# Optimization experiments

Hardware: AMD Instinct MI355X
Metric: run time of the kernel (lower is better)

## Reference

```python
import jax, jax.numpy as jnp
import numpy as np

P = 8          # patch_size
DIM = 256      # embed dim
HEADS = 8
HEAD_DIM = DIM // HEADS
CH = 3
PATCH_DIM = CH * P * P  # 192
INNER = int(4.0 * DIM)  # 1024
SCALE = HEAD_DIM ** -0.5


def sine_pos_embedding(n, c, dtype=jnp.float32):
    # standard 1D sinusoidal position encoding, shape (n, c)
    pos = jnp.arange(n, dtype=jnp.float32)[:, None]            # (n,1)
    div = jnp.exp(jnp.arange(0, c, 2, dtype=jnp.float32) * (-np.log(10000.0) / c))
    pe = jnp.zeros((n, c), dtype=jnp.float32)
    pe = pe.at[:, 0::2].set(jnp.sin(pos * div))
    pe = pe.at[:, 1::2].set(jnp.cos(pos * div))
    return pe.astype(dtype)


def patchify(x):
    # (B,C,H,W) -> (B, n, p1*p2*C), matching 'b c (h p1) (w p2) -> b (h w) (p1 p2 c)'
    B, C, H, W = x.shape
    hp, wp = H // P, W // P
    x = x.reshape(B, C, hp, P, wp, P)
    x = x.transpose(0, 2, 4, 3, 5, 1)        # (B, hp, wp, p1, p2, C)
    return x.reshape(B, hp * wp, P * P * C)


def unpatchify(x, hp, wp):
    # (B, n, p1*p2*C) -> (B, C, H, W)
    B = x.shape[0]
    x = x.reshape(B, hp, wp, P, P, CH)
    x = x.transpose(0, 5, 1, 3, 2, 4)        # (B, C, hp, p1, wp, p2)
    return x.reshape(B, CH, hp * P, wp * P)


def setup_inputs() -> dict:
    key = jax.random.key(0)
    ks = jax.random.split(key, 16)
    B, H, W = 8, 256, 256
    s = 0.02
    img0 = jax.random.normal(ks[0], (B, CH, H, W), dtype=jnp.float32)
    img1 = jax.random.normal(ks[1], (B, CH, H, W), dtype=jnp.float32)
    mask = jax.random.randint(ks[2], (B, 1, H, W), 0, 2).astype(jnp.float32)
    return {
        "img0": img0,
        "img1": img1,
        "mask": mask,
        "w_patch": jax.random.normal(ks[3], (PATCH_DIM, DIM), jnp.float32) * s,
        "b_patch": jnp.zeros((DIM,), jnp.float32),
        "w_kv": jax.random.normal(ks[4], (DIM, 2 * DIM), jnp.float32) * s,
        "b_kv": jnp.zeros((2 * DIM,), jnp.float32),
        "w_qv": jax.random.normal(ks[5], (DIM, 2 * DIM), jnp.float32) * s,
        "b_qv": jnp.zeros((2 * DIM,), jnp.float32),
        "w_fc1": jax.random.normal(ks[6], (DIM, INNER), jnp.float32) * s,
        "b_fc1": jnp.zeros((INNER,), jnp.float32),
        "w_fc2": jax.random.normal(ks[7], (INNER, PATCH_DIM), jnp.float32) * s,
        "b_fc2": jnp.zeros((PATCH_DIM,), jnp.float32),
    }


def reference(img0, img1, mask, w_patch, b_patch, w_kv, b_kv, w_qv, b_qv,
              w_fc1, b_fc1, w_fc2, b_fc2):
    B, C, H, W = img0.shape
    hp, wp = H // P, W // P
    n = hp * wp

    x0 = patchify(img0) @ w_patch + b_patch   # (B, n, dim)
    x1 = patchify(img1) @ w_patch + b_patch
    pe = sine_pos_embedding(n, DIM)
    x0 = x0 + pe
    x1 = x1 + pe

    # img0 -> k, v
    kv = (x0 @ w_kv + b_kv).reshape(B, n, 2, HEADS, HEAD_DIM)
    kv = kv.transpose(2, 0, 3, 1, 4)          # (2, B, heads, n, hd)
    k, v = kv[0], kv[1]

    # img1 -> q (v1 unused in forward, matching torch code)
    qv = (x1 @ w_qv + b_qv).reshape(B, n, 2, DIM).transpose(2, 0, 1, 3)
    q = qv[0].reshape(B, n, HEADS, HEAD_DIM).transpose(0, 2, 1, 3)  # (B, heads, n, hd)

    dots = jnp.einsum('bhqd,bhkd->bhqk', q, k) * SCALE  # (B, heads, n, n)

    # mask: (B,1,H,W) -> per-patch sum -> binary -> additive bias over key dim
    msum = mask.reshape(B, 1, hp, P, wp, P).sum(axis=(3, 5)).reshape(B, 1, n)
    bias = jnp.where(msum > 0, 0.0, -100.0)[:, :, None, :]  # (B,1,1,n)

    attn = jax.nn.softmax(dots + bias, axis=-1)
    out = jnp.einsum('bhqk,bhkd->bhqd', attn, v)
    out = out.transpose(0, 2, 1, 3).reshape(B, n, DIM)

    # mlp2: Linear -> GELU(exact) -> Linear
    h = jax.nn.gelu(out @ w_fc1 + b_fc1, approximate=False)
    res = h @ w_fc2 + b_fc2                   # (B, n, patch_dim)

    return unpatchify(res, hp, wp)            # (B, C, H, W)
```

## Files before the change

kernel.cpp:

```cpp
#include <hip/hip_runtime.h>
#include <cstdint>
#include <cstddef>

typedef __bf16 bf16_t;
typedef __bf16 bf16x8 __attribute__((ext_vector_type(8)));
typedef float f32x4 __attribute__((ext_vector_type(4)));

__device__ __forceinline__ void gload_lds16(const bf16_t* g, bf16_t* l) {
  __builtin_amdgcn_global_load_lds((const __attribute__((address_space(1))) void*)g,
                                   (__attribute__((address_space(3))) void*)l,
                                   16, 0, 0);
}

__device__ __forceinline__ f32x4 mfma16(bf16x8 a, bf16x8 b, f32x4 c) {
  return __builtin_amdgcn_mfma_f32_16x16x32_bf16(a, b, c, 0, 0, 0);
}

__global__ __launch_bounds__(256)
void prep_all(const float* __restrict__ img0, const float* __restrict__ img1,
              const float* __restrict__ mask,
              const float* __restrict__ wp, const float* __restrict__ wkv,
              const float* __restrict__ wqv, const float* __restrict__ wfc1,
              const float* __restrict__ wfc2,
              bf16_t* __restrict__ xp0, bf16_t* __restrict__ xp1,
              float* __restrict__ pe, float* __restrict__ bias,
              bf16_t* __restrict__ wpT, bf16_t* __restrict__ wkvT,
              bf16_t* __restrict__ wqT, bf16_t* __restrict__ wfc1T,
              bf16_t* __restrict__ wfc2T) {
  int bid = blockIdx.x, tid = threadIdx.x;
  if (bid < 1536) {
    int imgsel = bid >= 768;
    int t = (bid - (imgsel ? 768 : 0)) * 256 + tid;
    const float* img = imgsel ? img1 : img0;
    bf16_t* xp = imgsel ? xp1 : xp0;
    int wpp = t & 31, p1 = (t >> 5) & 7, hp = (t >> 8) & 31, rest = t >> 13;
    int b = rest / 3, c = rest - b * 3;
    const float* src = img + (((size_t)(b * 3 + c) * 256 + hp * 8 + p1) * 256 + wpp * 8);
    float4 v0 = *(const float4*)src;
    float4 v1 = *(const float4*)(src + 4);
    int row = b * 1024 + hp * 32 + wpp;
    bf16_t* dst = xp + (size_t)row * 192 + p1 * 24 + c;
    dst[0]  = (bf16_t)v0.x; dst[3]  = (bf16_t)v0.y; dst[6]  = (bf16_t)v0.z; dst[9]  = (bf16_t)v0.w;
    dst[12] = (bf16_t)v1.x; dst[15] = (bf16_t)v1.y; dst[18] = (bf16_t)v1.z; dst[21] = (bf16_t)v1.w;
  } else if (bid < 4544) {
    int g = (bid - 1536) * 256 + tid;
    if (g < 49152) {
      int idx = g; int n = idx / 192, k = idx - n * 192;
      wpT[idx] = (bf16_t)wp[k * 256 + n];
    } else if (g < 180224) {
      int idx = g - 49152; int n = idx >> 8, k = idx & 255;
      wkvT[idx] = (bf16_t)wkv[k * 512 + n];
    } else if (g < 245760) {
      int idx = g - 180224; int n = idx >> 8, k = idx & 255;
      wqT[idx] = (bf16_t)wqv[k * 512 + n];
    } else if (g < 507904) {
      int idx = g - 245760; int n = idx >> 8, k = idx & 255;
      wfc1T[idx] = (bf16_t)wfc1[k * 1024 + n];
    } else if (g < 770048) {
      int idx = g - 507904; int n = idx >> 10, k = idx & 1023;
      wfc2T[idx] = (n < 192) ? (bf16_t)wfc2[k * 192 + n] : (bf16_t)0.0f;
    }
  } else if (bid < 5568) {
    int t = bid - 4544, c = tid;
    int i2 = c & ~1;
    float div = expf((float)i2 * (-9.210340371976184f / 256.0f));
    float arg = (float)t * div;
    pe[t * 256 + c] = (c & 1) ? cosf(arg) : sinf(arg);
  } else {
    int g = (bid - 5568) * 256 + tid;
    int b = g >> 10, t = g & 1023, hp = t >> 5, wpp = t & 31;
    const float* mp = mask + ((size_t)b * 256 + hp * 8) * 256 + wpp * 8;
    float s = 0.f;
    #pragma unroll
    for (int p1 = 0; p1 < 8; p1++) {
      float4 a = *(const float4*)(mp + p1 * 256);
      float4 c = *(const float4*)(mp + p1 * 256 + 4);
      s += a.x + a.y + a.z + a.w + c.x + c.y + c.z + c.w;
    }
    bias[g] = (s > 0.f) ? 0.f : -100.f;
  }
}

template<int EPI>
__global__ __launch_bounds__(256)
void gemm_bt(const bf16_t* __restrict__ A_, const bf16_t* __restrict__ A2,
             const bf16_t* __restrict__ Bt_, const bf16_t* __restrict__ Bt2,
             int M, int N, int K,
             const float* __restrict__ bias_, const float* __restrict__ bias2,
             const float* __restrict__ pe,
             bf16_t* __restrict__ out_b, bf16_t* __restrict__ out_b2,
             bf16_t* __restrict__ out_b3, float* __restrict__ out_f) {
  __shared__ bf16_t alds[4 * 64 * 8];
  __shared__ bf16_t blds[4 * 128 * 8];
  const int tid = threadIdx.x;
  const int lane = tid & 63, wid = tid >> 6;
  const int ln15 = lane & 15, hi = lane >> 4;
  const int brow = blockIdx.x * 64;
  int bcol = blockIdx.y * 128;
  const bf16_t* A = A_;
  const bf16_t* Bt = Bt_;
  const float* bias = bias_;
  bool qpart = false;
  if (EPI == 0 && blockIdx.z) A = A2;
  if (EPI == 5 && blockIdx.y >= 4) {
    qpart = true; A = A2; Bt = Bt2; bias = bias2; bcol -= 512;
  }
  const int wr = wid >> 1, wc = wid & 1;

  f32x4 acc[2][4];
  #pragma unroll
  for (int m = 0; m < 2; m++)
    #pragma unroll
    for (int n = 0; n < 4; n++) acc[m][n] = (f32x4){0.f, 0.f, 0.f, 0.f};

  for (int k0 = 0; k0 < K; k0 += 32) {
    {
      int c = tid; int row = c & 63; int kb = c >> 6;
      const bf16_t* g = A + (size_t)(brow + row) * K + k0 + kb * 8;
      gload_lds16(g, &alds[(wid * 64) * 8]);
    }
    #pragma unroll
    for (int s = 0; s < 2; s++) {
      int c = tid + s * 256; int row = c & 127; int kb = c >> 7;
      const bf16_t* g = Bt + (size_t)(bcol + row) * K + k0 + kb * 8;
      gload_lds16(g, &blds[(wid * 64 + s * 256) * 8]);
    }
    __syncthreads();
    bf16x8 af[2], bfr[4];
    #pragma unroll
    for (int m = 0; m < 2; m++)
      af[m] = *(const bf16x8*)&alds[(hi * 64 + wr * 32 + m * 16 + ln15) * 8];
    #pragma unroll
    for (int n = 0; n < 4; n++)
      bfr[n] = *(const bf16x8*)&blds[(hi * 128 + wc * 64 + n * 16 + ln15) * 8];
    #pragma unroll
    for (int m = 0; m < 2; m++)
      #pragma unroll
      for (int n = 0; n < 4; n++)
        acc[m][n] = mfma16(af[m], bfr[n], acc[m][n]);
    __syncthreads();
  }

  #pragma unroll
  for (int m = 0; m < 2; m++) {
    #pragma unroll
    for (int n = 0; n < 4; n++) {
      #pragma unroll
      for (int r = 0; r < 4; r++) {
        int grow = brow + wr * 32 + m * 16 + hi * 4 + r;
        int gcol = bcol + wc * 64 + n * 16 + ln15;
        float v = acc[m][n][r];
        if (EPI == 0) {
          v += bias[gcol] + pe[(grow & 1023) * 256 + gcol];
          bf16_t* outx = blockIdx.z ? out_b2 : out_b;
          outx[(size_t)grow * N + gcol] = (bf16_t)v;
        } else if (EPI == 5) {
          v += bias[gcol];
          int b = grow >> 10, t = grow & 1023;
          if (!qpart) {
            if (gcol < 256) {
              int h = gcol >> 5, d = gcol & 31;
              out_b[(((size_t)(b * 8 + h) * 1024 + t) << 5) + d] = (bf16_t)v;
            } else {
              int c2 = gcol - 256; int h = c2 >> 5, d = c2 & 31;
              out_b2[(((size_t)(b * 8 + h) * 32 + d) << 10) + t] = (bf16_t)v;
            }
          } else {
            v *= 0.17677669529663687f;
            int h = gcol >> 5, d = gcol & 31;
            out_b3[(((size_t)(b * 8 + h) * 1024 + t) << 5) + d] = (bf16_t)v;
          }
        } else if (EPI == 3) {
          v += bias[gcol];
          float gg = 0.5f * v * (1.0f + erff(v * 0.7071067811865476f));
          out_b[(size_t)grow * N + gcol] = (bf16_t)gg;
        } else if (EPI == 4) {
          if (gcol < 192) {
            v += bias[gcol];
            int b = grow >> 10, t = grow & 1023;
            int hp = t >> 5, wpp = t & 31;
            int p = gcol / 3; int c = gcol - p * 3;
            int p1 = p >> 3, p2 = p & 7;
            out_f[(((size_t)(b * 3 + c) * 256 + hp * 8 + p1) * 256) + wpp * 8 + p2] = v;
          }
        }
      }
    }
  }
}

__global__ __launch_bounds__(256)
void attn_kernel(const bf16_t* __restrict__ q, const bf16_t* __restrict__ k,
                 const bf16_t* __restrict__ vt, const float* __restrict__ bias,
                 bf16_t* __restrict__ out) {
  __shared__ bf16_t plds[4 * 16 * 40];
  int tid = threadIdx.x;
  int lane = tid & 63, wid = tid >> 6, ln15 = lane & 15, hi = lane >> 4;
  int bh = blockIdx.x >> 4, qb = blockIdx.x & 15;
  int b = bh >> 3, h = bh & 7;
  int qrow = qb * 64 + wid * 16 + ln15;
  bf16x8 qf = *(const bf16x8*)(q + ((size_t)bh * 1024 + qrow) * 32 + hi * 8);
  const bf16_t* kbase = k + (size_t)bh * 32768;
  const bf16_t* vbase = vt + (size_t)bh * 32768;
  const float* bb = bias + b * 1024;
  bf16_t* pw = &plds[wid * 640];

  float lacc[4] = {0.f, 0.f, 0.f, 0.f};
  f32x4 o0 = (f32x4){0.f, 0.f, 0.f, 0.f}, o1 = o0;
  const f32x4 z = (f32x4){0.f, 0.f, 0.f, 0.f};

  for (int kt = 0; kt < 32; kt++) {
    int k0 = kt * 32;
    bf16x8 kf0 = *(const bf16x8*)(kbase + (size_t)(k0 + ln15) * 32 + hi * 8);
    bf16x8 kf1 = *(const bf16x8*)(kbase + (size_t)(k0 + 16 + ln15) * 32 + hi * 8);
    f32x4 s0 = mfma16(qf, kf0, z);
    f32x4 s1 = mfma16(qf, kf1, z);
    float bias0 = bb[k0 + ln15], bias1 = bb[k0 + 16 + ln15];
    #pragma unroll
    for (int r = 0; r < 4; r++) {
      float p0 = __expf(s0[r] + bias0);
      float p1 = __expf(s1[r] + bias1);
      lacc[r] += p0 + p1;
      pw[(hi * 4 + r) * 40 + ln15] = (bf16_t)p0;
      pw[(hi * 4 + r) * 40 + 16 + ln15] = (bf16_t)p1;
    }
    bf16x8 pf = *(const bf16x8*)&pw[ln15 * 40 + hi * 8];
    bf16x8 vf0 = *(const bf16x8*)(vbase + (size_t)ln15 * 1024 + k0 + hi * 8);
    bf16x8 vf1 = *(const bf16x8*)(vbase + (size_t)(16 + ln15) * 1024 + k0 + hi * 8);
    o0 = mfma16(pf, vf0, o0);
    o1 = mfma16(pf, vf1, o1);
  }

  float linv[4];
  #pragma unroll
  for (int r = 0; r < 4; r++) {
    float l = lacc[r];
    l += __shfl_xor(l, 1); l += __shfl_xor(l, 2);
    l += __shfl_xor(l, 4); l += __shfl_xor(l, 8);
    linv[r] = 1.f / l;
  }
  #pragma unroll
  for (int r = 0; r < 4; r++) {
    int qg = qb * 64 + wid * 16 + hi * 4 + r;
    size_t rowbase = ((size_t)b * 1024 + qg) * 256 + h * 32;
    out[rowbase + ln15] = (bf16_t)(o0[r] * linv[r]);
    out[rowbase + 16 + ln15] = (bf16_t)(o1[r] * linv[r]);
  }
}

extern "C" void kernel_launch(void* const* d_in, const int* in_sizes, int n_in,
                              void* d_out, int out_size, void* d_ws, size_t ws_size,
                              hipStream_t stream) {
  (void)in_sizes; (void)n_in; (void)out_size; (void)ws_size;
  const float* img0    = (const float*)d_in[0];
  const float* img1    = (const float*)d_in[1];
  const float* mask    = (const float*)d_in[2];
  const float* w_patch = (const float*)d_in[3];
  const float* b_patch = (const float*)d_in[4];
  const float* w_kv    = (const float*)d_in[5];
  const float* b_kv    = (const float*)d_in[6];
  const float* w_qv    = (const float*)d_in[7];
  const float* b_qv    = (const float*)d_in[8];
  const float* w_fc1   = (const float*)d_in[9];
  const float* b_fc1   = (const float*)d_in[10];
  const float* w_fc2   = (const float*)d_in[11];
  const float* b_fc2   = (const float*)d_in[12];
  float* out = (float*)d_out;

  char* ws = (char*)d_ws;
  float*  pe    = (float*)(ws + 0);
  float*  bias  = (float*)(ws + 1048576);
  bf16_t* wpT   = (bf16_t*)(ws + 1081344);
  bf16_t* wkvT  = (bf16_t*)(ws + 1179648);
  bf16_t* wqT   = (bf16_t*)(ws + 1441792);
  bf16_t* wfc1T = (bf16_t*)(ws + 1572864);
  bf16_t* wfc2T = (bf16_t*)(ws + 2097152);
  bf16_t* xp0   = (bf16_t*)(ws + 2621440);
  bf16_t* xp1   = (bf16_t*)(ws + 5767168);
  bf16_t* x0    = (bf16_t*)(ws + 8912896);
  bf16_t* x1    = (bf16_t*)(ws + 13107200);
  bf16_t* kbuf  = (bf16_t*)(ws + 17301504);
  bf16_t* vtbuf = (bf16_t*)(ws + 21495808);
  bf16_t* qbuf  = (bf16_t*)(ws + 25690112);
  bf16_t* aout  = (bf16_t*)(ws + 29884416);
  bf16_t* hbuf  = (bf16_t*)(ws + 34078720);

  prep_all<<<5600, 256, 0, stream>>>(img0, img1, mask, w_patch, w_kv, w_qv, w_fc1, w_fc2,
                                     xp0, xp1, pe, bias, wpT, wkvT, wqT, wfc1T, wfc2T);

  gemm_bt<0><<<dim3(128, 2, 2), 256, 0, stream>>>(xp0, xp1, wpT, nullptr, 8192, 256, 192,
                                                  b_patch, nullptr, pe, x0, x1, nullptr, nullptr);
  gemm_bt<5><<<dim3(128, 6), 256, 0, stream>>>(x0, x1, wkvT, wqT, 8192, 512, 256,
                                               b_kv, b_qv, nullptr, kbuf, vtbuf, qbuf, nullptr);

  attn_kernel<<<1024, 256, 0, stream>>>(qbuf, kbuf, vtbuf, bias, aout);

  gemm_bt<3><<<dim3(128, 8), 256, 0, stream>>>(aout, nullptr, wfc1T, nullptr, 8192, 1024, 256,
                                               b_fc1, nullptr, nullptr, hbuf, nullptr, nullptr, nullptr);
  gemm_bt<4><<<dim3(128, 2), 256, 0, stream>>>(hbuf, nullptr, wfc2T, nullptr, 8192, 256, 1024,
                                               b_fc2, nullptr, nullptr, nullptr, nullptr, nullptr, out);
}
```

Baseline: 143.4 us.

## Software-pipeline attention loads, transpose score MFMA, and narrow tiles for small GEMMs

The attention kernel now prefetches the next K/V/bias tile into registers while the current one is processed. It computes scores as K·Q so the mask bias enters through the MFMA accumulator, stores P with packed 4-wide LDS writes, and shortens the row-sum reduction to two shuffles. Block indices are remapped so consecutive blocks cover different heads. The GEMM kernel is templated on the N tile width, and the patch-embed and fc2 GEMMs use 64-wide tiles so each launches twice as many blocks, at the cost of more register pressure in attention and less reuse of A per block.

After: 145.1 us. No clear change (+1.1%).

```diff
diff --git a/kernel.cpp b/kernel.cpp
--- a/kernel.cpp
+++ b/kernel.cpp
@@ -3,6 +3,7 @@
 #include <cstddef>
 
 typedef __bf16 bf16_t;
+typedef __bf16 bf16x4 __attribute__((ext_vector_type(4)));
 typedef __bf16 bf16x8 __attribute__((ext_vector_type(8)));
 typedef float f32x4 __attribute__((ext_vector_type(4)));
 
@@ -81,7 +82,7 @@
   }
 }
 
-template<int EPI>
+template<int EPI, int BN>
 __global__ __launch_bounds__(256)
 void gemm_bt(const bf16_t* __restrict__ A_, const bf16_t* __restrict__ A2,
              const bf16_t* __restrict__ Bt_, const bf16_t* __restrict__ Bt2,
@@ -90,13 +91,14 @@
              const float* __restrict__ pe,
              bf16_t* __restrict__ out_b, bf16_t* __restrict__ out_b2,
              bf16_t* __restrict__ out_b3, float* __restrict__ out_f) {
+  constexpr int NF = BN / 32;
   __shared__ bf16_t alds[4 * 64 * 8];
-  __shared__ bf16_t blds[4 * 128 * 8];
+  __shared__ bf16_t blds[4 * BN * 8];
   const int tid = threadIdx.x;
   const int lane = tid & 63, wid = tid >> 6;
   const int ln15 = lane & 15, hi = lane >> 4;
   const int brow = blockIdx.x * 64;
-  int bcol = blockIdx.y * 128;
+  int bcol = blockIdx.y * BN;
   const bf16_t* A = A_;
   const bf16_t* Bt = Bt_;
   const float* bias = bias_;
@@ -107,11 +109,11 @@
   }
   const int wr = wid >> 1, wc = wid & 1;
 
-  f32x4 acc[2][4];
+  f32x4 acc[2][NF];
   #pragma unroll
   for (int m = 0; m < 2; m++)
     #pragma unroll
-    for (int n = 0; n < 4; n++) acc[m][n] = (f32x4){0.f, 0.f, 0.f, 0.f};
+    for (int n = 0; n < NF; n++) acc[m][n] = (f32x4){0.f, 0.f, 0.f, 0.f};
 
   for (int k0 = 0; k0 < K; k0 += 32) {
     {
@@ -120,23 +122,23 @@
       gload_lds16(g, &alds[(wid * 64) * 8]);
     }
     #pragma unroll
-    for (int s = 0; s < 2; s++) {
-      int c = tid + s * 256; int row = c & 127; int kb = c >> 7;
+    for (int s = 0; s < BN / 64; s++) {
+      int c = tid + s * 256; int row = c & (BN - 1); int kb = c / BN;
       const bf16_t* g = Bt + (size_t)(bcol + row) * K + k0 + kb * 8;
       gload_lds16(g, &blds[(wid * 64 + s * 256) * 8]);
     }
     __syncthreads();
-    bf16x8 af[2], bfr[4];
+    bf16x8 af[2], bfr[NF];
     #pragma unroll
     for (int m = 0; m < 2; m++)
       af[m] = *(const bf16x8*)&alds[(hi * 64 + wr * 32 + m * 16 + ln15) * 8];
     #pragma unroll
-    for (int n = 0; n < 4; n++)
-      bfr[n] = *(const bf16x8*)&blds[(hi * 128 + wc * 64 + n * 16 + ln15) * 8];
+    for (int n = 0; n < NF; n++)
+      bfr[n] = *(const bf16x8*)&blds[(hi * BN + wc * (BN / 2) + n * 16 + ln15) * 8];
     #pragma unroll
     for (int m = 0; m < 2; m++)
       #pragma unroll
-      for (int n = 0; n < 4; n++)
+      for (int n = 0; n < NF; n++)
         acc[m][n] = mfma16(af[m], bfr[n], acc[m][n]);
     __syncthreads();
   }
@@ -144,11 +146,11 @@
   #pragma unroll
   for (int m = 0; m < 2; m++) {
     #pragma unroll
-    for (int n = 0; n < 4; n++) {
+    for (int n = 0; n < NF; n++) {
       #pragma unroll
       for (int r = 0; r < 4; r++) {
         int grow = brow + wr * 32 + m * 16 + hi * 4 + r;
-        int gcol = bcol + wc * 64 + n * 16 + ln15;
+        int gcol = bcol + wc * (BN / 2) + n * 16 + ln15;
         float v = acc[m][n][r];
         if (EPI == 0) {
           v += bias[gcol] + pe[(grow & 1023) * 256 + gcol];
@@ -189,6 +191,38 @@
   }
 }
 
+__device__ __forceinline__ void attn_load(int kt, const bf16_t* kbase, const bf16_t* vbase,
+                                          const float* bb, int ln15, int hi,
+                                          bf16x8& kf0, bf16x8& kf1, bf16x8& vf0, bf16x8& vf1,
+                                          f32x4& ba0, f32x4& ba1) {
+  int k0 = kt * 32;
+  kf0 = *(const bf16x8*)(kbase + (size_t)(k0 + ln15) * 32 + hi * 8);
+  kf1 = *(const bf16x8*)(kbase + (size_t)(k0 + 16 + ln15) * 32 + hi * 8);
+  vf0 = *(const bf16x8*)(vbase + (size_t)ln15 * 1024 + k0 + hi * 8);
+  vf1 = *(const bf16x8*)(vbase + (size_t)(16 + ln15) * 1024 + k0 + hi * 8);
+  ba0 = *(const f32x4*)(bb + k0 + hi * 4);
+  ba1 = *(const f32x4*)(bb + k0 + 16 + hi * 4);
+}
+
+__device__ __forceinline__ void attn_step(bf16x8 kf0, bf16x8 kf1, bf16x8 vf0, bf16x8 vf1,
+                                          f32x4 ba0, f32x4 ba1, bf16x8 qf,
+                                          char* pwb, int ln15, int hi,
+                                          float& lsum, f32x4& o0, f32x4& o1) {
+  f32x4 s0 = mfma16(kf0, qf, ba0);
+  f32x4 s1 = mfma16(kf1, qf, ba1);
+  float e0 = __expf(s0[0]), e1 = __expf(s0[1]), e2 = __expf(s0[2]), e3 = __expf(s0[3]);
+  float f0 = __expf(s1[0]), f1 = __expf(s1[1]), f2 = __expf(s1[2]), f3 = __expf(s1[3]);
+  lsum += ((e0 + e1) + (e2 + e3)) + ((f0 + f1) + (f2 + f3));
+  bf16x4 pk0, pk1;
+  pk0[0] = (bf16_t)e0; pk0[1] = (bf16_t)e1; pk0[2] = (bf16_t)e2; pk0[3] = (bf16_t)e3;
+  pk1[0] = (bf16_t)f0; pk1[1] = (bf16_t)f1; pk1[2] = (bf16_t)f2; pk1[3] = (bf16_t)f3;
+  *(bf16x4*)(pwb + ln15 * 80 + hi * 8) = pk0;
+  *(bf16x4*)(pwb + ln15 * 80 + 32 + hi * 8) = pk1;
+  bf16x8 pf = *(const bf16x8*)(pwb + ln15 * 80 + hi * 16);
+  o0 = mfma16(pf, vf0, o0);
+  o1 = mfma16(pf, vf1, o1);
+}
+
 __global__ __launch_bounds__(256)
 void attn_kernel(const bf16_t* __restrict__ q, const bf16_t* __restrict__ k,
                  const bf16_t* __restrict__ vt, const float* __restrict__ bias,
@@ -196,55 +230,40 @@
   __shared__ bf16_t plds[4 * 16 * 40];
   int tid = threadIdx.x;
   int lane = tid & 63, wid = tid >> 6, ln15 = lane & 15, hi = lane >> 4;
-  int bh = blockIdx.x >> 4, qb = blockIdx.x & 15;
+  int x = blockIdx.x & 7, idx = blockIdx.x >> 3;
+  int qb = idx & 15;
+  int bh = ((idx >> 4) << 3) | x;
   int b = bh >> 3, h = bh & 7;
   int qrow = qb * 64 + wid * 16 + ln15;
   bf16x8 qf = *(const bf16x8*)(q + ((size_t)bh * 1024 + qrow) * 32 + hi * 8);
   const bf16_t* kbase = k + (size_t)bh * 32768;
   const bf16_t* vbase = vt + (size_t)bh * 32768;
   const float* bb = bias + b * 1024;
-  bf16_t* pw = &plds[wid * 640];
-
-  float lacc[4] = {0.f, 0.f, 0.f, 0.f};
+  char* pwb = (char*)&plds[wid * 640];
+
+  float lsum = 0.f;
   f32x4 o0 = (f32x4){0.f, 0.f, 0.f, 0.f}, o1 = o0;
-  const f32x4 z = (f32x4){0.f, 0.f, 0.f, 0.f};
-
-  for (int kt = 0; kt < 32; kt++) {
-    int k0 = kt * 32;
-    bf16x8 kf0 = *(const bf16x8*)(kbase + (size_t)(k0 + ln15) * 32 + hi * 8);
-    bf16x8 kf1 = *(const bf16x8*)(kbase + (size_t)(k0 + 16 + ln15) * 32 + hi * 8);
-    f32x4 s0 = mfma16(qf, kf0, z);
-    f32x4 s1 = mfma16(qf, kf1, z);
-    float bias0 = bb[k0 + ln15], bias1 = bb[k0 + 16 + ln15];
-    #pragma unroll
-    for (int r = 0; r < 4; r++) {
-      float p0 = __expf(s0[r] + bias0);
-      float p1 = __expf(s1[r] + bias1);
-      lacc[r] += p0 + p1;
-      pw[(hi * 4 + r) * 40 + ln15] = (bf16_t)p0;
-      pw[(hi * 4 + r) * 40 + 16 + ln15] = (bf16_t)p1;
-    }
-    bf16x8 pf = *(const bf16x8*)&pw[ln15 * 40 + hi * 8];
-    bf16x8 vf0 = *(const bf16x8*)(vbase + (size_t)ln15 * 1024 + k0 + hi * 8);
-    bf16x8 vf1 = *(const bf16x8*)(vbase + (size_t)(16 + ln15) * 1024 + k0 + hi * 8);
-    o0 = mfma16(pf, vf0, o0);
-    o1 = mfma16(pf, vf1, o1);
-  }
-
-  float linv[4];
+
+  bf16x8 ka0, ka1, va0, va1, kb0, kb1, vb0, vb1;
+  f32x4 aa0, aa1, ab0, ab1;
+  attn_load(0, kbase, vbase, bb, ln15, hi, ka0, ka1, va0, va1, aa0, aa1);
+  for (int kt = 0; kt < 32; kt += 2) {
+    attn_load(kt + 1, kbase, vbase, bb, ln15, hi, kb0, kb1, vb0, vb1, ab0, ab1);
+    attn_step(ka0, ka1, va0, va1, aa0, aa1, qf, pwb, ln15, hi, lsum, o0, o1);
+    int ktn = (kt + 2 < 32) ? kt + 2 : 31;
+    attn_load(ktn, kbase, vbase, bb, ln15, hi, ka0, ka1, va0, va1, aa0, aa1);
+    attn_step(kb0, kb1, vb0, vb1, ab0, ab1, qf, pwb, ln15, hi, lsum, o0, o1);
+  }
+
+  lsum += __shfl_xor(lsum, 16);
+  lsum += __shfl_xor(lsum, 32);
   #pragma unroll
   for (int r = 0; r < 4; r++) {
-    float l = lacc[r];
-    l += __shfl_xor(l, 1); l += __shfl_xor(l, 2);
-    l += __shfl_xor(l, 4); l += __shfl_xor(l, 8);
-    linv[r] = 1.f / l;
-  }
-  #pragma unroll
-  for (int r = 0; r < 4; r++) {
+    float linv = 1.f / __shfl(lsum, hi * 4 + r);
     int qg = qb * 64 + wid * 16 + hi * 4 + r;
     size_t rowbase = ((size_t)b * 1024 + qg) * 256 + h * 32;
-    out[rowbase + ln15] = (bf16_t)(o0[r] * linv[r]);
-    out[rowbase + 16 + ln15] = (bf16_t)(o1[r] * linv[r]);
+    out[rowbase + ln15] = (bf16_t)(o0[r] * linv);
+    out[rowbase + 16 + ln15] = (bf16_t)(o1[r] * linv);
   }
 }
 
@@ -288,15 +307,15 @@
   prep_all<<<5600, 256, 0, stream>>>(img0, img1, mask, w_patch, w_kv, w_qv, w_fc1, w_fc2,
                                      xp0, xp1, pe, bias, wpT, wkvT, wqT, wfc1T, wfc2T);
 
-  gemm_bt<0><<<dim3(128, 2, 2), 256, 0, stream>>>(xp0, xp1, wpT, nullptr, 8192, 256, 192,
-                                                  b_patch, nullptr, pe, x0, x1, nullptr, nullptr);
-  gemm_bt<5><<<dim3(128, 6), 256, 0, stream>>>(x0, x1, wkvT, wqT, 8192, 512, 256,
-                                               b_kv, b_qv, nullptr, kbuf, vtbuf, qbuf, nullptr);
+  gemm_bt<0, 64><<<dim3(128, 4, 2), 256, 0, stream>>>(xp0, xp1, wpT, nullptr, 8192, 256, 192,
+                                                      b_patch, nullptr, pe, x0, x1, nullptr, nullptr);
+  gemm_bt<5, 128><<<dim3(128, 6), 256, 0, stream>>>(x0, x1, wkvT, wqT, 8192, 512, 256,
+                                                    b_kv, b_qv, nullptr, kbuf, vtbuf, qbuf, nullptr);
 
   attn_kernel<<<1024, 256, 0, stream>>>(qbuf, kbuf, vtbuf, bias, aout);
 
-  gemm_bt<3><<<dim3(128, 8), 256, 0, stream>>>(aout, nullptr, wfc1T, nullptr, 8192, 1024, 256,
-                                               b_fc1, nullptr, nullptr, hbuf, nullptr, nullptr, nullptr);
-  gemm_bt<4><<<dim3(128, 2), 256, 0, stream>>>(hbuf, nullptr, wfc2T, nullptr, 8192, 256, 1024,
-                                               b_fc2, nullptr, nullptr, nullptr, nullptr, nullptr, out);
-}
+  gemm_bt<3, 128><<<dim3(128, 8), 256, 0, stream>>>(aout, nullptr, wfc1T, nullptr, 8192, 1024, 256,
+                                                    b_fc1, nullptr, nullptr, hbuf, nullptr, nullptr, nullptr);
+  gemm_bt<4, 64><<<dim3(128, 4), 256, 0, stream>>>(hbuf, nullptr, wfc2T, nullptr, 8192, 256, 1024,
+                                                   b_fc2, nullptr, nullptr, nullptr, nullptr, nullptr, out);
+}
```
